# Performance work log

Hardware: AMD Instinct MI355X
Metric: run time of the kernel (lower is better)

Reference implementation:

```python
import jax, jax.numpy as jnp
import numpy as np

B, N_PER_G, H, K, A, GNN_STEPS = 64, 100, 64, 5, 50, 3
N = B * N_PER_G  # total nodes


def _lin(key, din, dout):
    s = 1.0 / np.sqrt(din)
    kw, kb = jax.random.split(key)
    w = jax.random.uniform(kw, (din, dout), minval=-s, maxval=s, dtype=jnp.float32)
    b = jax.random.uniform(kb, (dout,), minval=-s, maxval=s, dtype=jnp.float32)
    return w, b


def setup_inputs() -> dict:
    key = jax.random.key(0)
    ks = jax.random.split(key, 16)
    # complete graph (no self loops) per batch graph
    i, j = np.meshgrid(np.arange(N_PER_G), np.arange(N_PER_G), indexing="ij")
    m = i != j
    s0, d0 = i[m], j[m]  # [n*(n-1)]
    offs = (np.arange(B) * N_PER_G)[:, None]
    src = jnp.asarray((s0[None, :] + offs).reshape(-1), dtype=jnp.int32)
    dst = jnp.asarray((d0[None, :] + offs).reshape(-1), dtype=jnp.int32)
    E = src.shape[0]
    e_type = jax.random.uniform(ks[0], (E, 2), dtype=jnp.float32)
    d = jax.random.uniform(ks[1], (E, 1), dtype=jnp.float32)
    label = jax.nn.one_hot(jax.random.randint(ks[2], (N,), 0, K), K, dtype=jnp.float32)
    actions = jax.random.randint(ks[3], (B * A, 2), 0, N_PER_G)
    l1_w, l1_b = _lin(ks[4], K, H)
    l2_w, l2_b = _lin(ks[5], H, H)
    t3_w, t3_b = _lin(ks[6], H, H)
    t4_wf, t4_b = _lin(ks[7], 1, H)
    t5_wf, t5_b = _lin(ks[8], H, 1)
    t6_w, t6_b = _lin(ks[9], H, H)
    t7_1_w, t7_1_b = _lin(ks[10], H, H)
    t7_2_w, t7_2_b = _lin(ks[11], H, H)
    t9_1_w, t9_1_b = _lin(ks[12], H, H)
    t9_2_w, t9_2_b = _lin(ks[13], H, H)
    return dict(label=label, e_type=e_type, d=d,
                l1_w=l1_w, l1_b=l1_b, l2_w=l2_w, l2_b=l2_b,
                t3_w=t3_w, t3_b=t3_b, t4_w=t4_wf[0], t4_b=t4_b,
                t5_w=t5_wf[:, 0], t5_b=t5_b, t6_w=t6_w, t6_b=t6_b,
                t7_1_w=t7_1_w, t7_1_b=t7_1_b, t7_2_w=t7_2_w, t7_2_b=t7_2_b,
                t9_1_w=t9_1_w, t9_1_b=t9_1_b, t9_2_w=t9_2_w, t9_2_b=t9_2_b,
                src=src, dst=dst, actions=actions)


def reference(label, e_type, d, l1_w, l1_b, l2_w, l2_b, t3_w, t3_b, t4_w, t4_b,
              t5_w, t5_b, t6_w, t6_b, t7_1_w, t7_1_b, t7_2_w, t7_2_b,
              t9_1_w, t9_1_b, t9_2_w, t9_2_b, src, dst, actions):
    e1 = e_type[:, 0]
    # n1_hd = h[src]*e1, n1_d = d*e1; bmm(n1_hd^T, n1_d) == sum over in-edges of h[src]*e1^2*d
    w_e = (e1 * e1) * d[:, 0]                              # [E]
    s_e = d[:, 0] * e1                                     # per-edge n1_d scalar [E]
    # sum_deg relu(t4(n1_d)) as edge-parallel relu + scatter-add
    t4_edge = jax.nn.relu(s_e[:, None] * t4_w[None, :] + t4_b)   # [E,H]
    t4_sum = jax.ops.segment_sum(t4_edge, dst, num_segments=N)   # [N,H]
    base = label @ l1_w + l1_b + t4_sum @ t3_w + t3_b            # constant across gnn steps
    h = jnp.zeros((N, H), dtype=label.dtype)
    for _ in range(GNN_STEPS):
        n1_h = jax.ops.segment_sum(h[src] * w_e[:, None], dst, num_segments=N)  # [N,H]
        h = jax.nn.relu(base + n1_h @ l2_w + l2_b)
    # readout (forward_): graph mean -> t6 stem; per-action node-pair branch
    stem = h.reshape(B, N_PER_G, H).mean(axis=1) @ t6_w + t6_b    # [B,H]
    h2 = h @ t7_1_w + t7_1_b                                      # [N,H]
    offs = jnp.repeat(jnp.arange(B, dtype=actions.dtype) * N_PER_G, A)
    a = actions + offs[:, None]                                   # global node ids [B*A,2]
    ha = h2[a[:, 0]] + h2[a[:, 1]]                                # [B*A,H]
    u = jax.nn.relu(jax.nn.relu(ha) @ t7_2_w + t7_2_b) @ t9_2_w + t9_2_b
    g_branch = jax.nn.relu(stem) @ t9_1_w + t9_1_b                # [B,H]
    q = jax.nn.relu(g_branch[:, None, :] + u.reshape(B, A, H))    # [B,A,H]
    Q_sa = q.reshape(B * A, H) @ t5_w + t5_b[0]                   # [B*A]
    return Q_sa
```

## Files before the change

### kernel.cpp

```cpp
#include <hip/hip_runtime.h>

#define HD 64
#define NPG 100
#define NGRP 64
#define NACT 50
#define EPG 9900
#define HSTRIDE 409600
#define FLAGSTRIDE 4096
#define MAGICF 0x9E3779B9u

typedef const float* fcp;

#define ACC_CHUNK(CK)                                                         \
    for (int ib = 0; ib < 7; ++ib) {                                          \
        const float h0 = hs[((CK) * 28 + 4 * ib + 0) * HD + hh];              \
        const float h1 = hs[((CK) * 28 + 4 * ib + 1) * HD + hh];              \
        const float h2 = hs[((CK) * 28 + 4 * ib + 2) * HD + hh];              \
        const float h3 = hs[((CK) * 28 + 4 * ib + 3) * HD + hh];              \
        _Pragma("unroll")                                                     \
        for (int m = 0; m < 4; ++m) {                                         \
            const int jl = w + 8 * m;                                         \
            if (jl < 25) {                                                    \
                const float4 wv =                                             \
                    *(const float4*)&w_pad[jl * 112 + (CK) * 28 + 4 * ib];    \
                acc[m] += wv.x * h0 + wv.y * h1 + wv.z * h2 + wv.w * h3;      \
            }                                                                 \
        }                                                                     \
    }

__global__ __launch_bounds__(512)
void k_dqnet(fcp label, fcp e_type, fcp dvec,
             fcp l1_w, fcp l1_b, fcp l2_w, fcp l2_b,
             fcp t3_w, fcp t3_b, fcp t4_w, fcp t4_b,
             fcp t5_w, fcp t5_b, fcp t6_w, fcp t6_b,
             fcp t7_1_w, fcp t7_1_b, fcp t7_2_w, fcp t7_2_b,
             fcp t9_1_w, fcp t9_1_b, fcp t9_2_w, fcp t9_2_b,
             const int* __restrict__ actions,
             float* __restrict__ hstg, unsigned* __restrict__ flags,
             float* __restrict__ out)
{
    const int g  = blockIdx.x >> 2;
    const int c  = blockIdx.x & 3;
    const int j0 = c * 25;
    const int t  = threadIdx.x;
    const int hh = t & 63;
    const int w  = t >> 6;

    __shared__ __align__(16) float s_ld[2500];
    __shared__ __align__(16) float w_pad[25 * 112];
    __shared__ __align__(16) float hs[112 * HD];
    __shared__ __align__(16) float t4s[25 * HD];
    __shared__ __align__(16) float awk[8 * HD];
    __shared__ float gbuf[HD];

    float l1r[5], lab[4][5];
    #pragma unroll
    for (int kk = 0; kk < 5; ++kk) l1r[kk] = l1_w[kk * HD + hh];
    #pragma unroll
    for (int m = 0; m < 4; ++m) {
        const int jl = w + 8 * m;
        #pragma unroll
        for (int kk = 0; kk < 5; ++kk)
            lab[m][kk] = (jl < 25) ? label[(g * NPG + j0 + jl) * 5 + kk] : 0.f;
    }
    const int acnt  = (c < 2) ? 13 : 12;
    const int abase = c * 12 + (c < 2 ? c : 2);
    int a0r[2], a1r[2];
    #pragma unroll
    for (int m = 0; m < 2; ++m) {
        const int al = w + 7 * m;
        a0r[m] = 0; a1r[m] = 0;
        if (w < 7 && al < acnt) {
            const int a = g * NACT + abase + al;
            a0r[m] = actions[a * 2 + 0];
            a1r[m] = actions[a * 2 + 1];
        }
        a0r[m] += 3 * (a0r[m] / 25);
        a1r[m] += 3 * (a1r[m] / 25);
    }

    for (int idx = t; idx < 768; idx += 512) {
        const int c2 = idx / 192, r = (idx % 192) / 64, ln = idx & 63;
        hs[(c2 * 28 + 25 + r) * HD + ln] = 0.f;
    }
    for (int idx = t; idx < 300; idx += 512) {
        const int jl = idx / 12, p = idx % 12;
        w_pad[jl * 112 + (p / 3) * 28 + 25 + (p % 3)] = 0.f;
    }

    const float2* et2 = (const float2*)e_type;
    const int ebase = g * EPG;
    for (int idx = t; idx < 2500; idx += 512) {
        const int i  = idx / 25;
        const int jl = idx - i * 25;
        const int j  = j0 + jl;
        float s = 0.f, wv = 0.f;
        if (i != j) {
            const int e = ebase + i * 99 + j - (j > i ? 1 : 0);
            const float e1 = et2[e].x;
            const float dd = dvec[e];
            s  = dd * e1;
            wv = e1 * e1 * dd;
        }
        s_ld[jl * 100 + i] = s;
        const int cb = i / 25;
        w_pad[jl * 112 + cb * 28 + (i - cb * 25)] = wv;
    }
    __syncthreads();

    const float w4  = t4_w[hh];
    const float b4  = t4_b[hh];
    const float rb4 = fmaxf(b4, 0.f);
    #pragma unroll
    for (int m = 0; m < 4; ++m) {
        const int jl = w + 8 * m;
        if (jl < 25) {
            float a0 = 0.f, a1 = 0.f, a2 = 0.f, a3 = 0.f;
            #pragma unroll 5
            for (int ib = 0; ib < 25; ++ib) {
                const float4 s4 = *(const float4*)&s_ld[jl * 100 + 4 * ib];
                a0 += fmaxf(s4.x * w4 + b4, 0.f);
                a1 += fmaxf(s4.y * w4 + b4, 0.f);
                a2 += fmaxf(s4.z * w4 + b4, 0.f);
                a3 += fmaxf(s4.w * w4 + b4, 0.f);
            }
            t4s[jl * HD + hh] = (a0 + a1) + (a2 + a3) - rb4;
        }
    }

    const float bb   = l1_b[hh] + t3_b[hh];
    const float l2bv = l2_b[hh];
    float basev[4];
    #pragma unroll
    for (int m = 0; m < 4; ++m) {
        float x = bb;
        #pragma unroll
        for (int kk = 0; kk < 5; ++kk) x += lab[m][kk] * l1r[kk];
        basev[m] = x;
    }
    for (int ib = 0; ib < 16; ++ib) {
        const float tw0 = t3_w[(4 * ib + 0) * HD + hh];
        const float tw1 = t3_w[(4 * ib + 1) * HD + hh];
        const float tw2 = t3_w[(4 * ib + 2) * HD + hh];
        const float tw3 = t3_w[(4 * ib + 3) * HD + hh];
        #pragma unroll
        for (int m = 0; m < 4; ++m) {
            const int jl = w + 8 * m;
            if (jl < 25) {
                const float4 x4 = *(const float4*)&t4s[jl * HD + 4 * ib];
                basev[m] += x4.x * tw0 + x4.y * tw1 + x4.z * tw2 + x4.w * tw3;
            }
        }
    }
    {
        #pragma unroll
        for (int m = 0; m < 4; ++m) {
            const int jl = w + 8 * m;
            if (jl < 25) {
                const float hv = fmaxf(basev[m] + l2bv, 0.f);
                hs[(c * 28 + jl) * HD + hh] = hv;
                __hip_atomic_store(hstg + (g * NPG + j0 + jl) * HD + hh, hv,
                                   __ATOMIC_RELAXED, __HIP_MEMORY_SCOPE_AGENT);
            }
        }
        asm volatile("s_waitcnt vmcnt(0)" ::: "memory");
        __syncthreads();
        if (t == 0)
            __hip_atomic_store(&flags[(g * 4 + c) * 16], MAGICF,
                               __ATOMIC_RELEASE, __HIP_MEMORY_SCOPE_AGENT);
    }

    const int c1 = (c + 1) & 3, c2i = (c + 2) & 3, c3 = (c + 3) & 3;
    #pragma unroll 1
    for (int step = 0; step < 2; ++step) {
        const float* buf = hstg + step * HSTRIDE;
        unsigned* flg = flags + step * FLAGSTRIDE;
        float* bufn = hstg + (step + 1) * HSTRIDE;
        unsigned* flgn = flags + (step + 1) * FLAGSTRIDE;

        float acc[4];
        #pragma unroll
        for (int m = 0; m < 4; ++m) acc[m] = 0.f;

        ACC_CHUNK(c)

        if (t == 0) {
            #pragma unroll
            for (int kk = 1; kk < 4; ++kk) {
                const int cs = (c + kk) & 3;
                while (__hip_atomic_load(&flg[(g * 4 + cs) * 16],
                                         __ATOMIC_RELAXED,
                                         __HIP_MEMORY_SCOPE_AGENT) != MAGICF)
                    __builtin_amdgcn_s_sleep(1);
            }
        }
        __syncthreads();

        const double* sb = (const double*)buf;
        const double* s1 = sb + (size_t)(g * NPG + c1 * 25) * 32;
        const double* s2 = sb + (size_t)(g * NPG + c2i * 25) * 32;
        const double* s3 = sb + (size_t)(g * NPG + c3 * 25) * 32;
        double* d1 = (double*)&hs[c1 * 28 * HD];
        double* d2 = (double*)&hs[c2i * 28 * HD];
        double* d3 = (double*)&hs[c3 * 28 * HD];
        const bool g2 = (t < 288);

        double a0 = __hip_atomic_load(s1 + t, __ATOMIC_RELAXED, __HIP_MEMORY_SCOPE_AGENT);
        double a1 = g2 ? __hip_atomic_load(s1 + 512 + t, __ATOMIC_RELAXED, __HIP_MEMORY_SCOPE_AGENT) : 0.0;
        double b0 = __hip_atomic_load(s2 + t, __ATOMIC_RELAXED, __HIP_MEMORY_SCOPE_AGENT);
        double b1 = g2 ? __hip_atomic_load(s2 + 512 + t, __ATOMIC_RELAXED, __HIP_MEMORY_SCOPE_AGENT) : 0.0;
        d1[t] = a0; if (g2) d1[512 + t] = a1;
        __syncthreads();
        double e0 = __hip_atomic_load(s3 + t, __ATOMIC_RELAXED, __HIP_MEMORY_SCOPE_AGENT);
        double e1 = g2 ? __hip_atomic_load(s3 + 512 + t, __ATOMIC_RELAXED, __HIP_MEMORY_SCOPE_AGENT) : 0.0;
        ACC_CHUNK(c1)
        d2[t] = b0; if (g2) d2[512 + t] = b1;
        __syncthreads();
        ACC_CHUNK(c2i)
        d3[t] = e0; if (g2) d3[512 + t] = e1;
        __syncthreads();
        ACC_CHUNK(c3)

        #pragma unroll
        for (int m = 0; m < 4; ++m) {
            const int jl = w + 8 * m;
            if (jl < 25) t4s[jl * HD + hh] = acc[m];
        }
        float v[4];
        #pragma unroll
        for (int m = 0; m < 4; ++m) v[m] = basev[m] + l2bv;
        for (int ib = 0; ib < 16; ++ib) {
            const float w0 = l2_w[(4 * ib + 0) * HD + hh];
            const float w1 = l2_w[(4 * ib + 1) * HD + hh];
            const float w2 = l2_w[(4 * ib + 2) * HD + hh];
            const float w3 = l2_w[(4 * ib + 3) * HD + hh];
            #pragma unroll
            for (int m = 0; m < 4; ++m) {
                const int jl = w + 8 * m;
                if (jl < 25) {
                    const float4 x4 = *(const float4*)&t4s[jl * HD + 4 * ib];
                    v[m] += x4.x * w0 + x4.y * w1 + x4.z * w2 + x4.w * w3;
                }
            }
        }
        #pragma unroll
        for (int m = 0; m < 4; ++m) {
            const int jl = w + 8 * m;
            if (jl < 25) {
                const float hv = fmaxf(v[m], 0.f);
                hs[(c * 28 + jl) * HD + hh] = hv;
                __hip_atomic_store(bufn + (g * NPG + j0 + jl) * HD + hh, hv,
                                   __ATOMIC_RELAXED, __HIP_MEMORY_SCOPE_AGENT);
            }
        }
        asm volatile("s_waitcnt vmcnt(0)" ::: "memory");
        __syncthreads();
        if (t == 0)
            __hip_atomic_store(&flgn[(g * 4 + c) * 16], MAGICF,
                               __ATOMIC_RELEASE, __HIP_MEMORY_SCOPE_AGENT);
    }

    {
        const float* buf2 = hstg + 2 * HSTRIDE;
        unsigned* flg2 = flags + 2 * FLAGSTRIDE;
        if (t == 0) {
            #pragma unroll
            for (int kk = 1; kk < 4; ++kk) {
                const int cs = (c + kk) & 3;
                while (__hip_atomic_load(&flg2[(g * 4 + cs) * 16],
                                         __ATOMIC_RELAXED,
                                         __HIP_MEMORY_SCOPE_AGENT) != MAGICF)
                    __builtin_amdgcn_s_sleep(1);
            }
        }
        __syncthreads();
        const bool g2 = (t < 288);
        #pragma unroll
        for (int kk = 1; kk < 4; ++kk) {
            const int ck = (c + kk) & 3;
            const double* s = (const double*)buf2 + (size_t)(g * NPG + ck * 25) * 32;
            double* d = (double*)&hs[ck * 28 * HD];
            d[t] = __hip_atomic_load(s + t, __ATOMIC_RELAXED, __HIP_MEMORY_SCOPE_AGENT);
            if (g2) d[512 + t] = __hip_atomic_load(s + 512 + t, __ATOMIC_RELAXED, __HIP_MEMORY_SCOPE_AGENT);
        }
        __syncthreads();
    }

    {
        float ml = 0.f;
        for (int j = w; j < 112; j += 8) ml += hs[j * HD + hh];
        awk[w * HD + hh] = ml;
    }
    float* hsum = s_ld;
    float* r1s  = s_ld + 13 * HD;
    #pragma unroll
    for (int m = 0; m < 2; ++m) {
        const int al = w + 7 * m;
        if (w < 7 && al < acnt)
            hsum[al * HD + hh] = hs[a0r[m] * HD + hh] + hs[a1r[m] * HD + hh];
    }
    __syncthreads();

    if (w == 7) {
        float ml = 0.f;
        #pragma unroll
        for (int ww = 0; ww < 8; ++ww) ml += awk[ww * HD + hh];
        ml *= (1.f / NPG);
        float s = t6_b[hh];
        #pragma unroll 8
        for (int q = 0; q < HD; ++q) s += __shfl(ml, q, 64) * t6_w[q * HD + hh];
        s = fmaxf(s, 0.f);
        float gb = t9_1_b[hh];
        #pragma unroll 8
        for (int q = 0; q < HD; ++q) gb += __shfl(s, q, 64) * t9_1_w[q * HD + hh];
        gbuf[hh] = gb;
    } else {
        const float b71 = 2.f * t7_1_b[hh];
        float r[2];
        r[0] = b71; r[1] = b71;
        for (int ib = 0; ib < 16; ++ib) {
            const float w0 = t7_1_w[(4 * ib + 0) * HD + hh];
            const float w1 = t7_1_w[(4 * ib + 1) * HD + hh];
            const float w2 = t7_1_w[(4 * ib + 2) * HD + hh];
            const float w3 = t7_1_w[(4 * ib + 3) * HD + hh];
            #pragma unroll
            for (int m = 0; m < 2; ++m) {
                const int al = w + 7 * m;
                if (al < acnt) {
                    const float4 x4 = *(const float4*)&hsum[al * HD + 4 * ib];
                    r[m] += x4.x * w0 + x4.y * w1 + x4.z * w2 + x4.w * w3;
                }
            }
        }
        #pragma unroll
        for (int m = 0; m < 2; ++m) {
            const int al = w + 7 * m;
            if (al < acnt) r1s[al * HD + hh] = fmaxf(r[m], 0.f);
        }
        const float b72 = t7_2_b[hh];
        r[0] = b72; r[1] = b72;
        for (int ib = 0; ib < 16; ++ib) {
            const float w0 = t7_2_w[(4 * ib + 0) * HD + hh];
            const float w1 = t7_2_w[(4 * ib + 1) * HD + hh];
            const float w2 = t7_2_w[(4 * ib + 2) * HD + hh];
            const float w3 = t7_2_w[(4 * ib + 3) * HD + hh];
            #pragma unroll
            for (int m = 0; m < 2; ++m) {
                const int al = w + 7 * m;
                if (al < acnt) {
                    const float4 x4 = *(const float4*)&r1s[al * HD + 4 * ib];
                    r[m] += x4.x * w0 + x4.y * w1 + x4.z * w2 + x4.w * w3;
                }
            }
        }
        #pragma unroll
        for (int m = 0; m < 2; ++m) {
            const int al = w + 7 * m;
            if (al < acnt) hsum[al * HD + hh] = fmaxf(r[m], 0.f);
        }
    }
    __syncthreads();

    if (w < 7) {
        const float b92  = t9_2_b[hh];
        const float t5wv = t5_w[hh];
        const float t5bv = t5_b[0];
        const float gbv  = gbuf[hh];
        float u[2];
        u[0] = b92; u[1] = b92;
        for (int ib = 0; ib < 16; ++ib) {
            const float w0 = t9_2_w[(4 * ib + 0) * HD + hh];
            const float w1 = t9_2_w[(4 * ib + 1) * HD + hh];
            const float w2 = t9_2_w[(4 * ib + 2) * HD + hh];
            const float w3 = t9_2_w[(4 * ib + 3) * HD + hh];
            #pragma unroll
            for (int m = 0; m < 2; ++m) {
                const int al = w + 7 * m;
                if (al < acnt) {
                    const float4 x4 = *(const float4*)&hsum[al * HD + 4 * ib];
                    u[m] += x4.x * w0 + x4.y * w1 + x4.z * w2 + x4.w * w3;
                }
            }
        }
        #pragma unroll
        for (int m = 0; m < 2; ++m) {
            const int al = w + 7 * m;
            float qv = fmaxf(gbv + u[m], 0.f) * t5wv;
            #pragma unroll
            for (int off = 32; off > 0; off >>= 1) qv += __shfl_xor(qv, off, 64);
            if (al < acnt && hh == 0) out[g * NACT + abase + al] = qv + t5bv;
        }
    }
}

extern "C" void kernel_launch(void* const* d_in, const int* in_sizes, int n_in,
                              void* d_out, int out_size, void* d_ws, size_t ws_size,
                              hipStream_t stream)
{
    fcp label  = (fcp)d_in[0];
    fcp e_type = (fcp)d_in[1];
    fcp dvec   = (fcp)d_in[2];
    fcp l1_w   = (fcp)d_in[3];
    fcp l1_b   = (fcp)d_in[4];
    fcp l2_w   = (fcp)d_in[5];
    fcp l2_b   = (fcp)d_in[6];
    fcp t3_w   = (fcp)d_in[7];
    fcp t3_b   = (fcp)d_in[8];
    fcp t4_w   = (fcp)d_in[9];
    fcp t4_b   = (fcp)d_in[10];
    fcp t5_w   = (fcp)d_in[11];
    fcp t5_b   = (fcp)d_in[12];
    fcp t6_w   = (fcp)d_in[13];
    fcp t6_b   = (fcp)d_in[14];
    fcp t7_1_w = (fcp)d_in[15];
    fcp t7_1_b = (fcp)d_in[16];
    fcp t7_2_w = (fcp)d_in[17];
    fcp t7_2_b = (fcp)d_in[18];
    fcp t9_1_w = (fcp)d_in[19];
    fcp t9_1_b = (fcp)d_in[20];
    fcp t9_2_w = (fcp)d_in[21];
    fcp t9_2_b = (fcp)d_in[22];
    const int* actions = (const int*)d_in[25];

    char* ws = (char*)d_ws;
    float*    hstg  = (float*)ws;
    unsigned* flags = (unsigned*)(ws + 3 * 1638400);

    k_dqnet<<<dim3(NGRP * 4), dim3(512), 0, stream>>>(
        label, e_type, dvec, l1_w, l1_b, l2_w, l2_b, t3_w, t3_b, t4_w, t4_b,
        t5_w, t5_b, t6_w, t6_b, t7_1_w, t7_1_b, t7_2_w, t7_2_b,
        t9_1_w, t9_1_b, t9_2_w, t9_2_b, actions, hstg, flags, (float*)d_out);
}
```

Measured before the change: 162.6 us.

## Compute first GNN step redundantly per block to remove one cross-block sync round

Each of the four blocks per graph now builds the full 100x100 edge matrix and computes base and first-step h for all 100 nodes locally. It then runs the second step's aggregation on its own chunk without waiting for the other blocks. This drops one global-memory exchange and flag-spin barrier, leaving two instead of three. The cost is four times more redundant prologue work per block (t4 sums, t3 matvec over all nodes) and more shared memory (10000-float s_full and 6400-float t4s), which may lower occupancy.

```diff
diff --git a/kernel.cpp b/kernel.cpp
--- a/kernel.cpp
+++ b/kernel.cpp
@@ -4,7 +4,6 @@
 #define NPG 100
 #define NGRP 64
 #define NACT 50
-#define EPG 9900
 #define HSTRIDE 409600
 #define FLAGSTRIDE 4096
 #define MAGICF 0x9E3779B9u
@@ -46,23 +45,16 @@
     const int hh = t & 63;
     const int w  = t >> 6;
 
-    __shared__ __align__(16) float s_ld[2500];
+    __shared__ __align__(16) float s_full[NPG * NPG];
     __shared__ __align__(16) float w_pad[25 * 112];
     __shared__ __align__(16) float hs[112 * HD];
-    __shared__ __align__(16) float t4s[25 * HD];
+    __shared__ __align__(16) float t4s[NPG * HD];
     __shared__ __align__(16) float awk[8 * HD];
     __shared__ float gbuf[HD];
 
-    float l1r[5], lab[4][5];
+    float l1r[5];
     #pragma unroll
     for (int kk = 0; kk < 5; ++kk) l1r[kk] = l1_w[kk * HD + hh];
-    #pragma unroll
-    for (int m = 0; m < 4; ++m) {
-        const int jl = w + 8 * m;
-        #pragma unroll
-        for (int kk = 0; kk < 5; ++kk)
-            lab[m][kk] = (jl < 25) ? label[(g * NPG + j0 + jl) * 5 + kk] : 0.f;
-    }
     const int acnt  = (c < 2) ? 13 : 12;
     const int abase = c * 12 + (c < 2 ? c : 2);
     int a0r[2], a1r[2];
@@ -89,11 +81,10 @@
     }
 
     const float2* et2 = (const float2*)e_type;
-    const int ebase = g * EPG;
-    for (int idx = t; idx < 2500; idx += 512) {
-        const int i  = idx / 25;
-        const int jl = idx - i * 25;
-        const int j  = j0 + jl;
+    const int ebase = g * 9900;
+    for (int idx = t; idx < NPG * NPG; idx += 512) {
+        const int i = idx / NPG;
+        const int j = idx - i * NPG;
         float s = 0.f, wv = 0.f;
         if (i != j) {
             const int e = ebase + i * 99 + j - (j > i ? 1 : 0);
@@ -102,86 +93,107 @@
             s  = dd * e1;
             wv = e1 * e1 * dd;
         }
-        s_ld[jl * 100 + i] = s;
-        const int cb = i / 25;
-        w_pad[jl * 112 + cb * 28 + (i - cb * 25)] = wv;
+        s_full[j * NPG + i] = s;
+        const int jl = j - j0;
+        if (jl >= 0 && jl < 25) {
+            const int cb = i / 25;
+            w_pad[jl * 112 + cb * 28 + (i - cb * 25)] = wv;
+        }
     }
     __syncthreads();
-
-    const float w4  = t4_w[hh];
-    const float b4  = t4_b[hh];
-    const float rb4 = fmaxf(b4, 0.f);
-    #pragma unroll
-    for (int m = 0; m < 4; ++m) {
-        const int jl = w + 8 * m;
-        if (jl < 25) {
-            float a0 = 0.f, a1 = 0.f, a2 = 0.f, a3 = 0.f;
-            #pragma unroll 5
-            for (int ib = 0; ib < 25; ++ib) {
-                const float4 s4 = *(const float4*)&s_ld[jl * 100 + 4 * ib];
-                a0 += fmaxf(s4.x * w4 + b4, 0.f);
-                a1 += fmaxf(s4.y * w4 + b4, 0.f);
-                a2 += fmaxf(s4.z * w4 + b4, 0.f);
-                a3 += fmaxf(s4.w * w4 + b4, 0.f);
-            }
-            t4s[jl * HD + hh] = (a0 + a1) + (a2 + a3) - rb4;
-        }
-    }
 
     const float bb   = l1_b[hh] + t3_b[hh];
     const float l2bv = l2_b[hh];
-    float basev[4];
-    #pragma unroll
-    for (int m = 0; m < 4; ++m) {
+    const float w4   = t4_w[hh];
+    const float b4   = t4_b[hh];
+    const float rb4  = fmaxf(b4, 0.f);
+    float basev[4] = {0.f, 0.f, 0.f, 0.f};
+    for (int m = 0; m < 13; ++m) {
+        const int k = w + 8 * m;
+        if (k >= NPG) break;
+        int r = j0 + k; if (r >= NPG) r -= NPG;
+        float a0 = 0.f, a1 = 0.f, a2 = 0.f, a3 = 0.f;
+        #pragma unroll 5
+        for (int ib = 0; ib < 25; ++ib) {
+            const float4 s4 = *(const float4*)&s_full[r * NPG + 4 * ib];
+            a0 += fmaxf(s4.x * w4 + b4, 0.f);
+            a1 += fmaxf(s4.y * w4 + b4, 0.f);
+            a2 += fmaxf(s4.z * w4 + b4, 0.f);
+            a3 += fmaxf(s4.w * w4 + b4, 0.f);
+        }
+        t4s[r * HD + hh] = (a0 + a1) + (a2 + a3) - rb4;
         float x = bb;
         #pragma unroll
-        for (int kk = 0; kk < 5; ++kk) x += lab[m][kk] * l1r[kk];
-        basev[m] = x;
-    }
-    for (int ib = 0; ib < 16; ++ib) {
-        const float tw0 = t3_w[(4 * ib + 0) * HD + hh];
-        const float tw1 = t3_w[(4 * ib + 1) * HD + hh];
-        const float tw2 = t3_w[(4 * ib + 2) * HD + hh];
-        const float tw3 = t3_w[(4 * ib + 3) * HD + hh];
+        for (int kk = 0; kk < 5; ++kk)
+            x += label[(g * NPG + r) * 5 + kk] * l1r[kk];
+        for (int ib = 0; ib < 16; ++ib) {
+            const float tw0 = t3_w[(4 * ib + 0) * HD + hh];
+            const float tw1 = t3_w[(4 * ib + 1) * HD + hh];
+            const float tw2 = t3_w[(4 * ib + 2) * HD + hh];
+            const float tw3 = t3_w[(4 * ib + 3) * HD + hh];
+            const float4 x4 = *(const float4*)&t4s[r * HD + 4 * ib];
+            x += x4.x * tw0 + x4.y * tw1 + x4.z * tw2 + x4.w * tw3;
+        }
+        if (m < 4 && k < 25) basev[m] = x;
+        const int pr = r + 3 * (r / 25);
+        hs[pr * HD + hh] = fmaxf(x + l2bv, 0.f);
+    }
+    __syncthreads();
+
+    {
+        float acc[4] = {0.f, 0.f, 0.f, 0.f};
+        ACC_CHUNK(0) ACC_CHUNK(1) ACC_CHUNK(2) ACC_CHUNK(3)
         #pragma unroll
         for (int m = 0; m < 4; ++m) {
             const int jl = w + 8 * m;
-            if (jl < 25) {
-                const float4 x4 = *(const float4*)&t4s[jl * HD + 4 * ib];
-                basev[m] += x4.x * tw0 + x4.y * tw1 + x4.z * tw2 + x4.w * tw3;
-            }
-        }
-    }
-    {
+            if (jl < 25) t4s[jl * HD + hh] = acc[m];
+        }
+        float v[4];
+        #pragma unroll
+        for (int m = 0; m < 4; ++m) v[m] = basev[m] + l2bv;
+        for (int ib = 0; ib < 16; ++ib) {
+            const float w0 = l2_w[(4 * ib + 0) * HD + hh];
+            const float w1 = l2_w[(4 * ib + 1) * HD + hh];
+            const float w2 = l2_w[(4 * ib + 2) * HD + hh];
+            const float w3 = l2_w[(4 * ib + 3) * HD + hh];
+            #pragma unroll
+            for (int m = 0; m < 4; ++m) {
+                const int jl = w + 8 * m;
+                if (jl < 25) {
+                    const float4 x4 = *(const float4*)&t4s[jl * HD + 4 * ib];
+                    v[m] += x4.x * w0 + x4.y * w1 + x4.z * w2 + x4.w * w3;
+                }
+            }
+        }
         #pragma unroll
         for (int m = 0; m < 4; ++m) {
             const int jl = w + 8 * m;
-            if (jl < 25) {
-                const float hv = fmaxf(basev[m] + l2bv, 0.f);
-                hs[(c * 28 + jl) * HD + hh] = hv;
-                __hip_atomic_store(hstg + (g * NPG + j0 + jl) * HD + hh, hv,
+            if (jl < 25)
+                __hip_atomic_store(hstg + (g * NPG + j0 + jl) * HD + hh,
+                                   fmaxf(v[m], 0.f),
                                    __ATOMIC_RELAXED, __HIP_MEMORY_SCOPE_AGENT);
-            }
         }
         asm volatile("s_waitcnt vmcnt(0)" ::: "memory");
         __syncthreads();
         if (t == 0)
             __hip_atomic_store(&flags[(g * 4 + c) * 16], MAGICF,
                                __ATOMIC_RELEASE, __HIP_MEMORY_SCOPE_AGENT);
+        #pragma unroll
+        for (int m = 0; m < 4; ++m) {
+            const int jl = w + 8 * m;
+            if (jl < 25) hs[(c * 28 + jl) * HD + hh] = fmaxf(v[m], 0.f);
+        }
+        __syncthreads();
     }
 
     const int c1 = (c + 1) & 3, c2i = (c + 2) & 3, c3 = (c + 3) & 3;
-    #pragma unroll 1
-    for (int step = 0; step < 2; ++step) {
-        const float* buf = hstg + step * HSTRIDE;
-        unsigned* flg = flags + step * FLAGSTRIDE;
-        float* bufn = hstg + (step + 1) * HSTRIDE;
-        unsigned* flgn = flags + (step + 1) * FLAGSTRIDE;
-
-        float acc[4];
-        #pragma unroll
-        for (int m = 0; m < 4; ++m) acc[m] = 0.f;
-
+    {
+        const float* buf = hstg;
+        unsigned* flg = flags;
+        float* bufn = hstg + HSTRIDE;
+        unsigned* flgn = flags + FLAGSTRIDE;
+
+        float acc[4] = {0.f, 0.f, 0.f, 0.f};
         ACC_CHUNK(c)
 
         if (t == 0) {
@@ -261,8 +273,8 @@
     }
 
     {
-        const float* buf2 = hstg + 2 * HSTRIDE;
-        unsigned* flg2 = flags + 2 * FLAGSTRIDE;
+        const float* buf2 = hstg + HSTRIDE;
+        unsigned* flg2 = flags + FLAGSTRIDE;
         if (t == 0) {
             #pragma unroll
             for (int kk = 1; kk < 4; ++kk) {
@@ -291,8 +303,8 @@
         for (int j = w; j < 112; j += 8) ml += hs[j * HD + hh];
         awk[w * HD + hh] = ml;
     }
-    float* hsum = s_ld;
-    float* r1s  = s_ld + 13 * HD;
+    float* hsum = s_full;
+    float* r1s  = s_full + 13 * HD;
     #pragma unroll
     for (int m = 0; m < 2; ++m) {
         const int al = w + 7 * m;
@@ -424,7 +436,7 @@
 
     char* ws = (char*)d_ws;
     float*    hstg  = (float*)ws;
-    unsigned* flags = (unsigned*)(ws + 3 * 1638400);
+    unsigned* flags = (unsigned*)(ws + 2 * 1638400);
 
     k_dqnet<<<dim3(NGRP * 4), dim3(512), 0, stream>>>(
         label, e_type, dvec, l1_w, l1_b, l2_w, l2_b, t3_w, t3_b, t4_w, t4_b,
```

New measurement: 181.3 us. 1.12x slower.
